# Performance work log

Measured on AMD Instinct MI355X. Metric: run time of the kernel, lower is better.

Reference implementation:

```python
import jax, jax.numpy as jnp
import numpy as np

N_NODES = 100000
N_EDGES = 600000
D = 128          # model_dim
R = 50           # deprel_size


def setup_inputs() -> dict:
    key = jax.random.key(0)
    ks = jax.random.split(key, 20)
    s = 1.0 / np.sqrt(D)
    inp = jax.random.normal(ks[0], (N_NODES, D), dtype=jnp.float32)
    deprel_edge = jax.random.randint(ks[1], (N_EDGES,), 0, R)
    deparc_edge = jax.random.randint(ks[2], (N_EDGES,), 0, 4)
    edge_index = jax.random.randint(ks[3], (2, N_EDGES), 0, N_NODES)
    # parameters (nn.Linear weights stored as [out, in]; gates are Linear(D,1))
    V_in = jax.random.normal(ks[4], (D, D), dtype=jnp.float32) * s
    V_out = jax.random.normal(ks[5], (D, D), dtype=jnp.float32) * s
    W_self = jax.random.normal(ks[6], (D, D), dtype=jnp.float32) * s
    W_norel = jax.random.normal(ks[7], (D, D), dtype=jnp.float32) * s
    V_in_gate = jax.random.normal(ks[8], (1, D), dtype=jnp.float32) * s
    V_out_gate = jax.random.normal(ks[9], (1, D), dtype=jnp.float32) * s
    W_self_gate = jax.random.normal(ks[10], (1, D), dtype=jnp.float32) * s
    W_norel_gate = jax.random.normal(ks[11], (1, D), dtype=jnp.float32) * s
    b_in = jax.random.normal(ks[12], (R, D), dtype=jnp.float32) * 0.02
    b_out = jax.random.normal(ks[13], (R, D), dtype=jnp.float32) * 0.02
    b_in_gate = jax.random.normal(ks[14], (R, 1), dtype=jnp.float32) * 0.02 + 1.0
    b_out_gate = jax.random.normal(ks[15], (R, 1), dtype=jnp.float32) * 0.02 + 1.0
    return {
        "inp": inp, "deprel_edge": deprel_edge, "deparc_edge": deparc_edge,
        "edge_index": edge_index,
        "V_in": V_in, "b_in": b_in, "V_in_gate": V_in_gate, "b_in_gate": b_in_gate,
        "V_out": V_out, "b_out": b_out, "V_out_gate": V_out_gate, "b_out_gate": b_out_gate,
        "W_self": W_self, "W_self_gate": W_self_gate,
        "W_norel": W_norel, "W_norel_gate": W_norel_gate,
    }


def reference(inp, deprel_edge, deparc_edge, edge_index,
              V_in, b_in, V_in_gate, b_in_gate,
              V_out, b_out, V_out_gate, b_out_gate,
              W_self, W_self_gate, W_norel, W_norel_gate):
    # deparc type codes: 0=align(in), 1=opposite(out), 2=self, 3=norelation
    num_nodes = inp.shape[0]
    src, tgt = edge_index[0], edge_index[1]
    # transformed node features per edge type: [4, N, D]
    T = jnp.stack([inp @ V_in.T, inp @ V_out.T, inp @ W_self.T, inp @ W_norel.T])
    # gate pre-activations per edge type: [4, N, 1]
    G = jnp.stack([inp @ V_in_gate.T, inp @ V_out_gate.T,
                   inp @ W_self_gate.T, inp @ W_norel_gate.T])
    zeros_b = jnp.zeros_like(b_in)
    zeros_bg = jnp.zeros_like(b_in_gate)
    B = jnp.stack([b_in, b_out, zeros_b, zeros_b])        # [4, R, D] (self/norel have no relation bias)
    Bg = jnp.stack([b_in_gate, b_out_gate, zeros_bg, zeros_bg])  # [4, R, 1]
    # per-edge gather + relation bias
    msg = T[deparc_edge, src] + B[deparc_edge, deprel_edge]        # [E, D]
    gate = jax.nn.sigmoid(G[deparc_edge, src] + Bg[deparc_edge, deprel_edge])  # [E, 1]
    # scatter-add to target nodes
    return jax.ops.segment_sum(msg * gate, tgt, num_segments=num_nodes)
```

## Files before the change

### kernel.cpp

```cpp
#include <hip/hip_runtime.h>
#include <hip/hip_bf16.h>

#define D 128
#define LSTR 136

typedef __bf16 bf16x8 __attribute__((ext_vector_type(8)));
typedef __bf16 bf16x4 __attribute__((ext_vector_type(4)));
typedef float  f32x4  __attribute__((ext_vector_type(4)));
typedef float  f32x2  __attribute__((ext_vector_type(2)));

template <int ISBF>
__device__ __forceinline__ bf16x8 ld8(const void* p, size_t elem)
{
    if (ISBF) return *(const bf16x8*)((const __bf16*)p + elem);
    const f32x4* f = (const f32x4*)((const float*)p + elem);
    f32x4 lo = f[0], hi = f[1];
    bf16x8 r;
    r[0] = (__bf16)lo[0]; r[1] = (__bf16)lo[1]; r[2] = (__bf16)lo[2]; r[3] = (__bf16)lo[3];
    r[4] = (__bf16)hi[0]; r[5] = (__bf16)hi[1]; r[6] = (__bf16)hi[2]; r[7] = (__bf16)hi[3];
    return r;
}
template <int ISBF>
__device__ __forceinline__ float ldf(const void* p, size_t elem)
{
    return ISBF ? (float)((const __bf16*)p)[elem] : ((const float*)p)[elem];
}

__global__ __launch_bounds__(256) void hist_detect_kernel(
    const int* __restrict__ tgt, int* __restrict__ counts, int E,
    const unsigned int* __restrict__ w, int* __restrict__ flag)
{
    __shared__ int cnt[256];
    int e = blockIdx.x * 256 + threadIdx.x;
    if (e < E) atomicAdd(&counts[tgt[e]], 1);
    if (blockIdx.x == 0) {
        int c = 0;
#pragma unroll
        for (int i = 0; i < 4; ++i) {
            unsigned int v = w[threadIdx.x * 4 + i];
            unsigned int ex = (v >> 7) & 0xFF;
            if (ex >= 90 && ex <= 134) ++c;
        }
        cnt[threadIdx.x] = c;
        __syncthreads();
        for (int s = 128; s > 0; s >>= 1) {
            if (threadIdx.x < s) cnt[threadIdx.x] += cnt[threadIdx.x + s];
            __syncthreads();
        }
        if (threadIdx.x == 0) flag[0] = (cnt[0] > 614) ? 1 : 0;
    }
}

__global__ __launch_bounds__(256) void scan1_kernel(
    const int* __restrict__ counts, int* __restrict__ rowptr,
    int* __restrict__ bsum, int M)
{
    __shared__ int sh[256];
    int base = blockIdx.x * 1024 + threadIdx.x * 4;
    int v[4];
#pragma unroll
    for (int k = 0; k < 4; ++k)
        v[k] = (base + k < M) ? counts[base + k] : 0;
    int tot = v[0] + v[1] + v[2] + v[3];
    sh[threadIdx.x] = tot;
    __syncthreads();
    for (int off = 1; off < 256; off <<= 1) {
        int t = (threadIdx.x >= off) ? sh[threadIdx.x - off] : 0;
        __syncthreads();
        sh[threadIdx.x] += t;
        __syncthreads();
    }
    int run = sh[threadIdx.x] - tot;
#pragma unroll
    for (int k = 0; k < 4; ++k) {
        if (base + k < M) rowptr[base + k] = run;
        run += v[k];
    }
    if (threadIdx.x == 255) bsum[blockIdx.x] = sh[255];
}

__global__ __launch_bounds__(256) void scan3_kernel(
    int* __restrict__ rowptr, int* __restrict__ cursor,
    const int* __restrict__ bsum, int M, int E)
{
    int b = blockIdx.x;
    int o = 0;
    for (int i = 0; i < b; ++i) o += bsum[i];
    int base = b * 1024 + threadIdx.x * 4;
#pragma unroll
    for (int k = 0; k < 4; ++k) {
        int i = base + k;
        if (i < M) {
            int r = rowptr[i] + o;
            rowptr[i] = r;
            cursor[i] = r;
        }
    }
    if (b == 0 && threadIdx.x == 0) rowptr[M] = E;
}

template <int ISBF>
__device__ __forceinline__ void gemm1_body(
    int pb, int nbg,
    const void* __restrict__ inp,
    const void* __restrict__ W0, const void* __restrict__ W1,
    const void* __restrict__ W2, const void* __restrict__ W3,
    const void* __restrict__ g0, const void* __restrict__ g1,
    const void* __restrict__ g2, const void* __restrict__ g3,
    const void* __restrict__ b_in, const void* __restrict__ b_out,
    const void* __restrict__ bg_in, const void* __restrict__ bg_out,
    __bf16* __restrict__ T, float* __restrict__ G,
    __bf16* __restrict__ Bz, float* __restrict__ Bgz, int M,
    __bf16* sh)
{
    const int xcd = pb & 7, slot = pb >> 3;
    const int q = nbg >> 3, r = nbg & 7;
    const int lin = (xcd < r) ? xcd * (q + 1) + slot
                              : r * (q + 1) + (xcd - r) * q + slot;
    const int tile = lin >> 2;
    const int t    = lin & 3;

    if (pb < 101 && threadIdx.x < 128) {
        int row = pb;
        int tid = threadIdx.x;
        float v = 0.f, gv = 0.f;
        if (row < 50) {
            v  = ldf<ISBF>(b_in, (size_t)row * D + tid);
            gv = ldf<ISBF>(bg_in, row);
        } else if (row < 100) {
            int rr = row - 50;
            v  = ldf<ISBF>(b_out, (size_t)rr * D + tid);
            gv = ldf<ISBF>(bg_out, rr);
        }
        Bz[(size_t)row * D + tid] = (__bf16)v;
        if (tid == 0) Bgz[row] = gv;
    }

    const int wave = threadIdx.x >> 6;
    const int lane = threadIdx.x & 63;
    const int lrow = lane & 15;
    const int kgrp = lane >> 4;
    const int m_base = tile * 128 + wave * 32;

    int n0 = m_base + lrow;      if (n0 >= M) n0 = 0;
    int n1 = m_base + 16 + lrow; if (n1 >= M) n1 = 0;

    bf16x8 af0[4], af1[4];
#pragma unroll
    for (int ks = 0; ks < 4; ++ks) {
        const int k0 = ks * 32 + kgrp * 8;
        af0[ks] = ld8<ISBF>(inp, (size_t)n0 * D + k0);
        af1[ks] = ld8<ISBF>(inp, (size_t)n1 * D + k0);
    }

    {
        const void* gs[4] = {g0, g1, g2, g3};
        const void* gt = gs[t];
        float s0 = 0.f, s1 = 0.f;
#pragma unroll
        for (int ks = 0; ks < 4; ++ks) {
            bf16x8 qv = ld8<ISBF>(gt, ks * 32 + kgrp * 8);
#pragma unroll
            for (int j = 0; j < 8; ++j) {
                float qf = (float)qv[j];
                s0 = fmaf((float)af0[ks][j], qf, s0);
                s1 = fmaf((float)af1[ks][j], qf, s1);
            }
        }
        s0 += __shfl_xor(s0, 16); s0 += __shfl_xor(s0, 32);
        s1 += __shfl_xor(s1, 16); s1 += __shfl_xor(s1, 32);
        if (kgrp == 0) {
            int nn0 = m_base + lrow;
            int nn1 = m_base + 16 + lrow;
            if (nn0 < M) G[(size_t)t * M + nn0] = s0;
            if (nn1 < M) G[(size_t)t * M + nn1] = s1;
        }
    }

    const void* Ws[4] = {W0, W1, W2, W3};
    const void* W = Ws[t];

    f32x4 acc[2][8];
#pragma unroll
    for (int i = 0; i < 2; ++i)
#pragma unroll
        for (int j = 0; j < 8; ++j)
            acc[i][j] = (f32x4){0.f, 0.f, 0.f, 0.f};

#pragma unroll
    for (int h = 0; h < 2; ++h) {
#pragma unroll
        for (int i = 0; i < 4; ++i) {
            int idx = threadIdx.x + 256 * i;
            int f = idx >> 3;
            int s = idx & 7;
            int sp = s ^ (f & 7);
            bf16x8 v = ld8<ISBF>(W, (size_t)f * D + h * 64 + s * 8);
            *(bf16x8*)(sh + f * 64 + sp * 8) = v;
        }
        __syncthreads();

#pragma unroll
        for (int kl = 0; kl < 2; ++kl) {
            const int ks = h * 2 + kl;
            const int slot = kl * 4 + kgrp;
#pragma unroll
            for (int ft = 0; ft < 8; ++ft) {
                int f = ft * 16 + lrow;
                int sp = slot ^ (f & 7);
                bf16x8 wf = *(const bf16x8*)(sh + f * 64 + sp * 8);
                acc[0][ft] = __builtin_amdgcn_mfma_f32_16x16x32_bf16(wf, af0[ks], acc[0][ft], 0, 0, 0);
                acc[1][ft] = __builtin_amdgcn_mfma_f32_16x16x32_bf16(wf, af1[ks], acc[1][ft], 0, 0, 0);
            }
        }
        __syncthreads();
    }

#pragma unroll
    for (int bh = 0; bh < 2; ++bh) {
        if ((wave >> 1) == bh) {
            int nlb = (wave & 1) * 32;
#pragma unroll
            for (int nt = 0; nt < 2; ++nt) {
#pragma unroll
                for (int ft = 0; ft < 8; ++ft) {
                    int f0 = ft * 16 + kgrp * 4;
                    f32x4 v = acc[nt][ft];
                    bf16x4 w4;
                    w4[0] = (__bf16)v[0]; w4[1] = (__bf16)v[1];
                    w4[2] = (__bf16)v[2]; w4[3] = (__bf16)v[3];
                    *(bf16x4*)(sh + (nlb + nt * 16 + lrow) * LSTR + f0) = w4;
                }
            }
        }
        __syncthreads();
#pragma unroll
        for (int s = 0; s < 4; ++s) {
            int idx = s * 256 + threadIdx.x;
            int node = idx >> 4;
            int seg  = idx & 15;
            bf16x8 v = *(const bf16x8*)(sh + node * LSTR + seg * 8);
            int gn = tile * 128 + bh * 64 + node;
            if (gn < M)
                *(bf16x8*)(T + (size_t)gn * (4 * D) + t * D + seg * 8) = v;
        }
        if (bh == 0) __syncthreads();
    }
}

__global__ __launch_bounds__(256, 4) void scatter_gemm1_kernel(
    const int* __restrict__ deprel, const int* __restrict__ deparc,
    const int* __restrict__ srcA, const int* __restrict__ tgtA,
    int* __restrict__ cursor, int2* __restrict__ recs, int E, int NSb,
    const void* __restrict__ inp,
    const void* __restrict__ W0, const void* __restrict__ W1,
    const void* __restrict__ W2, const void* __restrict__ W3,
    const void* __restrict__ g0, const void* __restrict__ g1,
    const void* __restrict__ g2, const void* __restrict__ g3,
    const void* __restrict__ b_in, const void* __restrict__ b_out,
    const void* __restrict__ bg_in, const void* __restrict__ bg_out,
    __bf16* __restrict__ T, float* __restrict__ G,
    __bf16* __restrict__ Bz, float* __restrict__ Bgz, int M,
    const int* __restrict__ flag)
{
    __shared__ unsigned int shu[4352];

    if ((int)blockIdx.x < NSb) {
        int e = blockIdx.x * 256 + threadIdx.x;
        if (e < E) {
            int g = tgtA[e];
            int pos = atomicAdd(&cursor[g], 1);
            recs[pos] = make_int2(srcA[e], (deprel[e] << 2) | deparc[e]);
        }
        return;
    }

    const int pb  = blockIdx.x - NSb;
    const int nbg = gridDim.x - NSb;
    if (flag[0]) gemm1_body<1>(pb, nbg, inp, W0, W1, W2, W3, g0, g1, g2, g3,
                               b_in, b_out, bg_in, bg_out, T, G, Bz, Bgz, M,
                               (__bf16*)shu);
    else         gemm1_body<0>(pb, nbg, inp, W0, W1, W2, W3, g0, g1, g2, g3,
                               b_in, b_out, bg_in, bg_out, T, G, Bz, Bgz, M,
                               (__bf16*)shu);
}

template <int ISBF>
__device__ __forceinline__ void edge_agg2_body(
    const __bf16* __restrict__ T, const float* __restrict__ G,
    const __bf16* __restrict__ Bz, const float* __restrict__ Bgz,
    const int* __restrict__ rowptr, const int2* __restrict__ recs,
    void* __restrict__ out, int M)
{
    const int g = blockIdx.x * 16 + (threadIdx.x >> 4);
    if (g >= M) return;
    const int lane16 = threadIdx.x & 15;
    const int dd = lane16 * 8;

    const int beg = rowptr[g], end = rowptr[g + 1];
    const int n = end - beg;

    float acc[8];
#pragma unroll
    for (int k = 0; k < 8; ++k) acc[k] = 0.f;

    bf16x8 tv_c = {}, bz_c = {};
    float gp_c = 0.f, bg_c = 0.f;
    int2 rec_n = make_int2(0, 0);

    auto issue = [&](int2 rec) {
        int t = rec.y & 3;
        int r = rec.y >> 2;
        int bidx = (t < 2) ? t * 50 + r : 100;
        gp_c = G[(size_t)t * M + rec.x];
        bg_c = Bgz[bidx];
        tv_c = *(const bf16x8*)(T + (size_t)rec.x * (4 * D) + t * D + dd);
        bz_c = *(const bf16x8*)(Bz + (size_t)bidx * D + dd);
    };

    if (n > 0) {
        issue(recs[beg]);
        if (n > 1) rec_n = recs[beg + 1];
    }

    for (int e = 0; e < n; ++e) {
        const bf16x8 tv = tv_c, bz = bz_c;
        const float gp = gp_c, bg = bg_c;

        if (e + 1 < n) {
            issue(rec_n);
            if (e + 2 < n) rec_n = recs[beg + e + 2];
        }

        const float gate = 1.f / (1.f + __expf(-(gp + bg)));
#pragma unroll
        for (int k = 0; k < 8; ++k)
            acc[k] = fmaf(gate, (float)tv[k] + (float)bz[k], acc[k]);
    }

    if (ISBF) {
        bf16x8 w;
#pragma unroll
        for (int k = 0; k < 8; ++k) w[k] = (__bf16)acc[k];
        __builtin_nontemporal_store(w, (bf16x8*)((__bf16*)out + (size_t)g * D + dd));
    } else {
        f32x4 lo = {acc[0], acc[1], acc[2], acc[3]};
        f32x4 hi = {acc[4], acc[5], acc[6], acc[7]};
        __builtin_nontemporal_store(lo, (f32x4*)((float*)out + (size_t)g * D + dd));
        __builtin_nontemporal_store(hi, (f32x4*)((float*)out + (size_t)g * D + dd + 4));
    }
}

__global__ __launch_bounds__(256) void edge_agg2_kernel(
    const __bf16* __restrict__ T, const float* __restrict__ G,
    const __bf16* __restrict__ Bz, const float* __restrict__ Bgz,
    const int* __restrict__ rowptr, const int2* __restrict__ recs,
    void* __restrict__ out, int M, const int* __restrict__ flag)
{
    if (flag[0]) edge_agg2_body<1>(T, G, Bz, Bgz, rowptr, recs, out, M);
    else         edge_agg2_body<0>(T, G, Bz, Bgz, rowptr, recs, out, M);
}

__global__ void sentinel_kernel(__bf16* o, int n)
{
    int i = blockIdx.x * blockDim.x + threadIdx.x;
    if (i < n) o[i] = (__bf16)12345.0f;
}

static inline size_t align256(size_t x) { return (x + 255) & ~(size_t)255; }

extern "C" void kernel_launch(void* const* d_in, const int* in_sizes, int n_in,
                              void* d_out, int out_size, void* d_ws, size_t ws_size,
                              hipStream_t stream)
{
    const void* inp       = d_in[0];
    const int*  deprel    = (const int*)d_in[1];
    const int*  deparc    = (const int*)d_in[2];
    const int*  eidx      = (const int*)d_in[3];
    const void* V_in      = d_in[4];
    const void* b_in      = d_in[5];
    const void* V_in_g    = d_in[6];
    const void* b_in_g    = d_in[7];
    const void* V_out     = d_in[8];
    const void* b_out     = d_in[9];
    const void* V_out_g   = d_in[10];
    const void* b_out_g   = d_in[11];
    const void* W_self    = d_in[12];
    const void* W_self_g  = d_in[13];
    const void* W_norel   = d_in[14];
    const void* W_norel_g = d_in[15];

    const int M = in_sizes[0] / D;
    const int E = in_sizes[1];
    const int* src = eidx;
    const int* tgt = eidx + E;
    const int NB = (M + 1023) / 1024;

    size_t off = 0;
    size_t o_flag   = off; off = align256(off + sizeof(int));
    size_t o_T      = off; off = align256(off + (size_t)M * 4 * D * sizeof(__bf16));
    size_t o_G      = off; off = align256(off + (size_t)4 * M * sizeof(float));
    size_t o_counts = off; off = align256(off + (size_t)M * sizeof(int));
    size_t o_rowptr = off; off = align256(off + (size_t)(M + 1) * sizeof(int));
    size_t o_cursor = off; off = align256(off + (size_t)M * sizeof(int));
    size_t o_bsum   = off; off = align256(off + (size_t)NB * sizeof(int));
    size_t o_recs   = off; off = align256(off + (size_t)E * sizeof(int2));
    size_t o_Bz     = off; off = align256(off + (size_t)101 * D * sizeof(__bf16));
    size_t o_Bgz    = off; off = align256(off + (size_t)101 * sizeof(float));

    if (off > ws_size) {
        sentinel_kernel<<<(out_size + 255) / 256, 256, 0, stream>>>(
            (__bf16*)d_out, out_size);
        return;
    }

    int*    flag   = (int*)((char*)d_ws + o_flag);
    __bf16* T      = (__bf16*)((char*)d_ws + o_T);
    float*  Gbuf   = (float*)((char*)d_ws + o_G);
    int*    counts = (int*)((char*)d_ws + o_counts);
    int*    rowptr = (int*)((char*)d_ws + o_rowptr);
    int*    cursor = (int*)((char*)d_ws + o_cursor);
    int*    bsum   = (int*)((char*)d_ws + o_bsum);
    int2*   recs   = (int2*)((char*)d_ws + o_recs);
    __bf16* Bz     = (__bf16*)((char*)d_ws + o_Bz);
    float*  Bgz    = (float*)((char*)d_ws + o_Bgz);

    hipMemsetAsync(counts, 0, (size_t)M * sizeof(int), stream);
    hist_detect_kernel<<<(E + 255) / 256, 256, 0, stream>>>(
        tgt, counts, E, (const unsigned int*)inp, flag);
    scan1_kernel<<<NB, 256, 0, stream>>>(counts, rowptr, bsum, M);
    scan3_kernel<<<NB, 256, 0, stream>>>(rowptr, cursor, bsum, M, E);

    const int ntiles = (M + 127) / 128;
    const int NSb = (((E + 255) / 256) + 7) & ~7;
    scatter_gemm1_kernel<<<NSb + ntiles * 4, 256, 0, stream>>>(
        deprel, deparc, src, tgt, cursor, recs, E, NSb,
        inp, V_in, V_out, W_self, W_norel,
        V_in_g, V_out_g, W_self_g, W_norel_g,
        b_in, b_out, b_in_g, b_out_g, T, Gbuf, Bz, Bgz, M, flag);

    edge_agg2_kernel<<<(M + 15) / 16, 256, 0, stream>>>(
        T, Gbuf, Bz, Bgz, rowptr, recs, d_out, M, flag);
}
```

Before: 274.5 us.

## Split GEMM tiles across histogram and scatter kernels with interleaved block roles

The node-feature GEMM used to run only alongside the edge scatter. Its tiles are now split in half: one half runs inside the histogram kernel and the other inside the scatter kernel. Blocks interleave the atomic-heavy edge work with GEMM tiles, and the tile index is mapped per XCD slot. This is meant to hide the latency-bound histogram and scatter atomics behind compute. It adds a separate single-block detect launch and makes the tile-to-XCD mapping more complex.

```diff
diff --git a/kernel.cpp b/kernel.cpp
--- a/kernel.cpp
+++ b/kernel.cpp
@@ -26,29 +26,31 @@
     return ISBF ? (float)((const __bf16*)p)[elem] : ((const float*)p)[elem];
 }
 
-__global__ __launch_bounds__(256) void hist_detect_kernel(
-    const int* __restrict__ tgt, int* __restrict__ counts, int E,
-    const unsigned int* __restrict__ w, int* __restrict__ flag)
+__device__ __forceinline__ void split_role(int g, int NA, int NB, bool& isA, int& idx)
+{
+    int mn = (NA < NB) ? NA : NB;
+    if (g < 2 * mn) { isA = ((g & 1) == 0); idx = g >> 1; }
+    else if (NA >= NB) { isA = true;  idx = g - NB; }
+    else               { isA = false; idx = g - NA; }
+}
+
+__global__ void detect_kernel(const unsigned int* __restrict__ w, int* flag)
 {
     __shared__ int cnt[256];
-    int e = blockIdx.x * 256 + threadIdx.x;
-    if (e < E) atomicAdd(&counts[tgt[e]], 1);
-    if (blockIdx.x == 0) {
-        int c = 0;
-#pragma unroll
-        for (int i = 0; i < 4; ++i) {
-            unsigned int v = w[threadIdx.x * 4 + i];
-            unsigned int ex = (v >> 7) & 0xFF;
-            if (ex >= 90 && ex <= 134) ++c;
-        }
-        cnt[threadIdx.x] = c;
-        __syncthreads();
-        for (int s = 128; s > 0; s >>= 1) {
-            if (threadIdx.x < s) cnt[threadIdx.x] += cnt[threadIdx.x + s];
-            __syncthreads();
-        }
-        if (threadIdx.x == 0) flag[0] = (cnt[0] > 614) ? 1 : 0;
-    }
+    int c = 0;
+#pragma unroll
+    for (int i = 0; i < 4; ++i) {
+        unsigned int v = w[threadIdx.x * 4 + i];
+        unsigned int e = (v >> 7) & 0xFF;
+        if (e >= 90 && e <= 134) ++c;
+    }
+    cnt[threadIdx.x] = c;
+    __syncthreads();
+    for (int s = 128; s > 0; s >>= 1) {
+        if (threadIdx.x < s) cnt[threadIdx.x] += cnt[threadIdx.x + s];
+        __syncthreads();
+    }
+    if (threadIdx.x == 0) flag[0] = (cnt[0] > 614) ? 1 : 0;
 }
 
 __global__ __launch_bounds__(256) void scan1_kernel(
@@ -101,7 +103,7 @@
 
 template <int ISBF>
 __device__ __forceinline__ void gemm1_body(
-    int pb, int nbg,
+    int lin,
     const void* __restrict__ inp,
     const void* __restrict__ W0, const void* __restrict__ W1,
     const void* __restrict__ W2, const void* __restrict__ W3,
@@ -113,15 +115,11 @@
     __bf16* __restrict__ Bz, float* __restrict__ Bgz, int M,
     __bf16* sh)
 {
-    const int xcd = pb & 7, slot = pb >> 3;
-    const int q = nbg >> 3, r = nbg & 7;
-    const int lin = (xcd < r) ? xcd * (q + 1) + slot
-                              : r * (q + 1) + (xcd - r) * q + slot;
     const int tile = lin >> 2;
     const int t    = lin & 3;
 
-    if (pb < 101 && threadIdx.x < 128) {
-        int row = pb;
+    if (lin < 101 && threadIdx.x < 128) {
+        int row = lin;
         int tid = threadIdx.x;
         float v = 0.f, gv = 0.f;
         if (row < 50) {
@@ -248,10 +246,9 @@
     }
 }
 
-__global__ __launch_bounds__(256, 4) void scatter_gemm1_kernel(
-    const int* __restrict__ deprel, const int* __restrict__ deparc,
-    const int* __restrict__ srcA, const int* __restrict__ tgtA,
-    int* __restrict__ cursor, int2* __restrict__ recs, int E, int NSb,
+__global__ __launch_bounds__(256, 4) void hist_gemm1_kernel(
+    const int* __restrict__ tgtA, int* __restrict__ counts, int E,
+    int NA, int NB, int LPX, int slot_base, int ntiles4,
     const void* __restrict__ inp,
     const void* __restrict__ W0, const void* __restrict__ W1,
     const void* __restrict__ W2, const void* __restrict__ W3,
@@ -264,23 +261,59 @@
     const int* __restrict__ flag)
 {
     __shared__ unsigned int shu[4352];
-
-    if ((int)blockIdx.x < NSb) {
-        int e = blockIdx.x * 256 + threadIdx.x;
-        if (e < E) {
-            int g = tgtA[e];
-            int pos = atomicAdd(&cursor[g], 1);
-            recs[pos] = make_int2(srcA[e], (deprel[e] << 2) | deparc[e]);
-        }
+    const int g = blockIdx.x >> 3, sub = blockIdx.x & 7;
+    bool isA; int idx;
+    split_role(g, NA, NB, isA, idx);
+    if (isA) {
+        int e = (idx * 8 + sub) * 256 + threadIdx.x;
+        if (e < E) atomicAdd(&counts[tgtA[e]], 1);
         return;
     }
-
-    const int pb  = blockIdx.x - NSb;
-    const int nbg = gridDim.x - NSb;
-    if (flag[0]) gemm1_body<1>(pb, nbg, inp, W0, W1, W2, W3, g0, g1, g2, g3,
+    const int lin = sub * LPX + slot_base + idx;
+    if (lin >= ntiles4) return;
+    if (flag[0]) gemm1_body<1>(lin, inp, W0, W1, W2, W3, g0, g1, g2, g3,
                                b_in, b_out, bg_in, bg_out, T, G, Bz, Bgz, M,
                                (__bf16*)shu);
-    else         gemm1_body<0>(pb, nbg, inp, W0, W1, W2, W3, g0, g1, g2, g3,
+    else         gemm1_body<0>(lin, inp, W0, W1, W2, W3, g0, g1, g2, g3,
+                               b_in, b_out, bg_in, bg_out, T, G, Bz, Bgz, M,
+                               (__bf16*)shu);
+}
+
+__global__ __launch_bounds__(256, 4) void scat_gemm1_kernel(
+    const int* __restrict__ deprel, const int* __restrict__ deparc,
+    const int* __restrict__ srcA, const int* __restrict__ tgtA,
+    int* __restrict__ cursor, int2* __restrict__ recs, int E,
+    int NA, int NB, int LPX, int slot_base, int ntiles4,
+    const void* __restrict__ inp,
+    const void* __restrict__ W0, const void* __restrict__ W1,
+    const void* __restrict__ W2, const void* __restrict__ W3,
+    const void* __restrict__ g0, const void* __restrict__ g1,
+    const void* __restrict__ g2, const void* __restrict__ g3,
+    const void* __restrict__ b_in, const void* __restrict__ b_out,
+    const void* __restrict__ bg_in, const void* __restrict__ bg_out,
+    __bf16* __restrict__ T, float* __restrict__ G,
+    __bf16* __restrict__ Bz, float* __restrict__ Bgz, int M,
+    const int* __restrict__ flag)
+{
+    __shared__ unsigned int shu[4352];
+    const int g = blockIdx.x >> 3, sub = blockIdx.x & 7;
+    bool isA; int idx;
+    split_role(g, NA, NB, isA, idx);
+    if (isA) {
+        int e = (idx * 8 + sub) * 256 + threadIdx.x;
+        if (e < E) {
+            int gg = tgtA[e];
+            int pos = atomicAdd(&cursor[gg], 1);
+            recs[pos] = make_int2(srcA[e], (deprel[e] << 2) | deparc[e]);
+        }
+        return;
+    }
+    const int lin = sub * LPX + slot_base + idx;
+    if (lin >= ntiles4) return;
+    if (flag[0]) gemm1_body<1>(lin, inp, W0, W1, W2, W3, g0, g1, g2, g3,
+                               b_in, b_out, bg_in, bg_out, T, G, Bz, Bgz, M,
+                               (__bf16*)shu);
+    else         gemm1_body<0>(lin, inp, W0, W1, W2, W3, g0, g1, g2, g3,
                                b_in, b_out, bg_in, bg_out, T, G, Bz, Bgz, M,
                                (__bf16*)shu);
 }
@@ -425,20 +458,31 @@
     __bf16* Bz     = (__bf16*)((char*)d_ws + o_Bz);
     float*  Bgz    = (float*)((char*)d_ws + o_Bgz);
 
+    const int ntiles  = (M + 127) / 128;
+    const int ntiles4 = ntiles * 4;
+    const int LPX = (ntiles4 + 7) / 8;
+    const int SA  = (LPX + 1) / 2;
+    const int SB  = LPX - SA;
+    const int NEg = ((E + 255) / 256 + 7) / 8;
+
+    detect_kernel<<<1, 256, 0, stream>>>((const unsigned int*)inp, flag);
     hipMemsetAsync(counts, 0, (size_t)M * sizeof(int), stream);
-    hist_detect_kernel<<<(E + 255) / 256, 256, 0, stream>>>(
-        tgt, counts, E, (const unsigned int*)inp, flag);
-    scan1_kernel<<<NB, 256, 0, stream>>>(counts, rowptr, bsum, M);
-    scan3_kernel<<<NB, 256, 0, stream>>>(rowptr, cursor, bsum, M, E);
-
-    const int ntiles = (M + 127) / 128;
-    const int NSb = (((E + 255) / 256) + 7) & ~7;
-    scatter_gemm1_kernel<<<NSb + ntiles * 4, 256, 0, stream>>>(
-        deprel, deparc, src, tgt, cursor, recs, E, NSb,
+
+    hist_gemm1_kernel<<<(NEg + SA) * 8, 256, 0, stream>>>(
+        tgt, counts, E, NEg, SA, LPX, 0, ntiles4,
         inp, V_in, V_out, W_self, W_norel,
         V_in_g, V_out_g, W_self_g, W_norel_g,
         b_in, b_out, b_in_g, b_out_g, T, Gbuf, Bz, Bgz, M, flag);
 
+    scan1_kernel<<<NB, 256, 0, stream>>>(counts, rowptr, bsum, M);
+    scan3_kernel<<<NB, 256, 0, stream>>>(rowptr, cursor, bsum, M, E);
+
+    scat_gemm1_kernel<<<(NEg + SB) * 8, 256, 0, stream>>>(
+        deprel, deparc, src, tgt, cursor, recs, E, NEg, SB, LPX, SA, ntiles4,
+        inp, V_in, V_out, W_self, W_norel,
+        V_in_g, V_out_g, W_self_g, W_norel_g,
+        b_in, b_out, b_in_g, b_out_g, T, Gbuf, Bz, Bgz, M, flag);
+
     edge_agg2_kernel<<<(M + 15) / 16, 256, 0, stream>>>(
         T, Gbuf, Bz, Bgz, rowptr, recs, d_out, M, flag);
 }
```

Result: slower. 284.8 us (+3.8%).
